# Kernel tuning notes

Measured on AMD Instinct MI355X. Metric: run time of the kernel, lower is better.

Reference implementation:

```python
import jax, jax.numpy as jnp
import numpy as np

V, E, M, L = 32000, 1024, 4096, 4  # vocab, embed_dim, mlp_dim, mlp_layers
B, S = 4, 2048                      # batch, seq_len


def setup_inputs() -> dict:
    key = jax.random.key(0)
    ks = jax.random.split(key, 7)
    init = lambda k, shape, fan: (jax.random.normal(k, shape, jnp.float32) / np.sqrt(fan).astype(np.float32))
    return {
        "x": jax.random.randint(ks[0], (B, S), 0, V),
        "emb": init(ks[1], (V, E), E),
        "Wq": init(ks[2], (E, E), E), "bq": jnp.zeros((E,), jnp.float32),
        "Wk": init(ks[3], (E, E), E), "bk": jnp.zeros((E,), jnp.float32),
        "Wv": init(ks[4], (E, E), E), "bv": jnp.zeros((E,), jnp.float32),
        "W1": init(ks[5], (L, E, M), E), "b1": jnp.zeros((L, M), jnp.float32),
        "W2": init(ks[6], (L, M, E), M), "b2": jnp.zeros((L, E), jnp.float32),
    }


def reference(x, emb, Wq, bq, Wk, bk, Wv, bv, W1, b1, W2, b2):
    h = emb[x]                                   # [B,S,E]
    q = h @ Wq + bq
    k = h @ Wk + bk
    v = h @ Wv + bv
    scale = 1.0 / np.sqrt(E).astype(np.float32)
    scores = jnp.einsum("bse,bte->bst", q, k) * scale   # [B,S,S]
    # torch.triu(ones, diagonal=0): keep upper triangle incl. diagonal (anti-causal/suffix mask)
    mask = jnp.triu(jnp.ones((S, S), dtype=bool), k=0)
    scores = jnp.where(mask, scores, -jnp.inf)
    w = jax.nn.softmax(scores, axis=-1)
    h = jax.nn.relu(jnp.einsum("bst,bte->bse", w, v))
    for i in range(L):
        h = jax.nn.relu(h @ W1[i] + b1[i])
        h = jax.nn.relu(h @ W2[i] + b2[i])
    return h
```

## Files before the change

### kernel.cpp

```cpp
#include <hip/hip_runtime.h>
#include <hip/hip_bf16.h>

#define EDIM 1024
#define MDIM 4096
#define SEQ  2048
#define NB   4
#define ROWS 8192

#define BM 128
#define BN 128
#define BK 32

typedef short bh8 __attribute__((ext_vector_type(8)));
typedef float f32x16 __attribute__((ext_vector_type(16)));

__device__ __forceinline__ float bf2f(unsigned short u) {
    return __uint_as_float(((unsigned int)u) << 16);
}
__device__ __forceinline__ unsigned short f2bf(float f) {
    unsigned int u = __float_as_uint(f);
    u += 0x7FFFu + ((u >> 16) & 1u);
    return (unsigned short)(u >> 16);
}
__device__ __forceinline__ void splitf(float v, unsigned short& h, unsigned short& l) {
    h = f2bf(v);
    l = f2bf(v - __uint_as_float(((unsigned int)h) << 16));
}
__device__ __forceinline__ void ld4f(const float* __restrict__ p, float* d) {
    const float4 v = *reinterpret_cast<const float4*>(p);
    d[0] = v.x; d[1] = v.y; d[2] = v.z; d[3] = v.w;
}
__device__ __forceinline__ void ld4h(const unsigned short* __restrict__ p, float* d) {
    const ushort4 v = *reinterpret_cast<const ushort4*>(p);
    d[0] = bf2f(v.x); d[1] = bf2f(v.y); d[2] = bf2f(v.z); d[3] = bf2f(v.w);
}

__device__ __forceinline__ long long tidx8(int n, int k, int KD16) {
    return ((((long long)(n >> 5) * KD16 + (k >> 4)) * 2 + ((k >> 3) & 1)) * 32 + (n & 31)) * 8;
}

__global__ __launch_bounds__(64)
void sniff_k(const unsigned int* __restrict__ w, int* __restrict__ flag) {
    int ok = 0;
    const int base = threadIdx.x * 32;
#pragma unroll
    for (int i = 0; i < 32; ++i) {
        const unsigned int v = w[base + i];
        const unsigned int lo = v & 0xFFFFu, hi = v >> 16;
        const unsigned int el = (lo >> 7) & 0xFF, eh = (hi >> 7) & 0xFF;
        const bool okl = (lo == 0u) || (el >= 0x30u && el <= 0x7Eu);
        const bool okh = (hi == 0u) || (eh >= 0x30u && eh <= 0x7Eu);
        ok += (okl && okh) ? 1 : 0;
    }
#pragma unroll
    for (int off = 32; off > 0; off >>= 1) ok += __shfl_down(ok, off);
    if (threadIdx.x == 0) *flag = (ok > 1400) ? 1 : 0;
}

__global__ __launch_bounds__(256)
void gather_k(const int* __restrict__ x, const void* __restrict__ emb,
              float* __restrict__ h, const int* __restrict__ flagp) {
    const int bf = *flagp;
    const long long row = blockIdx.x;
    const int idx = x[row];
    const long long off = (long long)idx * EDIM + threadIdx.x * 4;
    float d[4];
    if (bf) ld4h((const unsigned short*)emb + off, d);
    else    ld4f((const float*)emb + off, d);
    *reinterpret_cast<float4*>(h + row * EDIM + threadIdx.x * 4)
        = make_float4(d[0], d[1], d[2], d[3]);
}

__global__ __launch_bounds__(256)
void splitrows_tiled_k(const float* __restrict__ in, unsigned short* __restrict__ oh,
                       unsigned short* __restrict__ ol) {
    const int rr = blockIdx.x * 2 + (threadIdx.x >> 7);
    const int chunk = threadIdx.x & 127;
    const int k = chunk * 8;
    const float* p = in + (long long)rr * 1024 + k;
    float d[8];
    ld4f(p, d); ld4f(p + 4, d + 4);
    unsigned short h[8], l[8];
#pragma unroll
    for (int j = 0; j < 8; ++j) splitf(d[j], h[j], l[j]);
    const int z = rr >> 11, n = rr & 2047;
    const long long o = (long long)z * (2048LL * 1024) + tidx8(n, k, 64);
    uint4 hv, lv;
    hv.x = (unsigned)h[0] | ((unsigned)h[1] << 16);
    hv.y = (unsigned)h[2] | ((unsigned)h[3] << 16);
    hv.z = (unsigned)h[4] | ((unsigned)h[5] << 16);
    hv.w = (unsigned)h[6] | ((unsigned)h[7] << 16);
    lv.x = (unsigned)l[0] | ((unsigned)l[1] << 16);
    lv.y = (unsigned)l[2] | ((unsigned)l[3] << 16);
    lv.z = (unsigned)l[4] | ((unsigned)l[5] << 16);
    lv.w = (unsigned)l[6] | ((unsigned)l[7] << 16);
    *reinterpret_cast<uint4*>(oh + o) = hv;
    *reinterpret_cast<uint4*>(ol + o) = lv;
}

__global__ __launch_bounds__(256)
void splitT_tiled_k(const void* __restrict__ in, unsigned short* __restrict__ oh,
                    unsigned short* __restrict__ ol, int Kd, int Nd,
                    long long inOff, long long zIn, long long zOut,
                    const int* __restrict__ flagp, int bF) {
    const int bf = bF ? *flagp : 0;
    const long long ib = inOff + (long long)blockIdx.z * zIn;
    const long long ob = (long long)blockIdx.z * zOut;
    const int k0 = blockIdx.y * 32, n0 = blockIdx.x * 32;
    const int KD16 = Kd >> 4;
    __shared__ float t[32][33];
    const int c = threadIdx.x & 31, r0 = threadIdx.x >> 5;
#pragma unroll
    for (int i = 0; i < 4; ++i) {
        const int r = r0 + i * 8;
        const long long off = ib + (long long)(k0 + r) * Nd + n0 + c;
        t[r][c] = bf ? bf2f(((const unsigned short*)in)[off]) : ((const float*)in)[off];
    }
    __syncthreads();
#pragma unroll
    for (int i = 0; i < 4; ++i) {
        const int r = r0 + i * 8;
        const float v = t[c][r];
        unsigned short hh, ll;
        splitf(v, hh, ll);
        const int n = n0 + r, k = k0 + c;
        const long long oo = ob + tidx8(n, k, KD16) + (k & 7);
        oh[oo] = hh; ol[oo] = ll;
    }
}

template<bool BIAS, bool RELU, bool MASK>
__global__ __launch_bounds__(256, 3)
void mgemm_k(const float* __restrict__ A,
             const unsigned short* __restrict__ Bh,
             const unsigned short* __restrict__ Bl,
             const void* __restrict__ biasv, void* __restrict__ Cv,
             int M, int N, int K,
             long long sA, long long sB, long long sC,
             long long biasBase, float scale,
             const int* __restrict__ flagp, int bF, int cF) {
    const int flag = *flagp;
    const int bfBias = bF ? flag : 0;
    const int bfC = cF ? flag : 0;

    A  += (long long)blockIdx.z * sA;
    Bh += (long long)blockIdx.z * sB;
    Bl += (long long)blockIdx.z * sB;
    const long long zC = (long long)blockIdx.z * sC;

    const int GX = gridDim.x;
    const int f = blockIdx.y * GX + blockIdx.x;
    const int gxpc = GX >> 3;
    const int xcd = f & 7, p = f >> 3;
    const int bx = xcd * gxpc + (p % gxpc);
    const int by = p / gxpc;
    const int brow = by * BM, bcol = bx * BN;

    const int tid = threadIdx.x;
    const int lane = tid & 63, wave = tid >> 6;
    const int wr = wave >> 1, wc = wave & 1;
    const int l31 = lane & 31, lhi = lane >> 5;

    if (MASK && (bcol + BN - 1 < brow)) {
#pragma unroll
        for (int mi = 0; mi < 2; ++mi) {
            const int rbase = brow + wr * 64 + mi * 32 + 4 * lhi;
#pragma unroll
            for (int ni = 0; ni < 2; ++ni) {
                const int c = bcol + wc * 64 + ni * 32 + l31;
#pragma unroll
                for (int e = 0; e < 16; ++e) {
                    const int r = rbase + (e & 3) + 8 * (e >> 2);
                    ((float*)Cv)[zC + (long long)r * N + c] = -1e30f;
                }
            }
        }
        return;
    }

    __shared__ __align__(16) unsigned short Ash[2][BM * BK];
    __shared__ __align__(16) unsigned short Asl[2][BM * BK];

    f32x16 acc[2][2];
#pragma unroll
    for (int a = 0; a < 2; ++a)
#pragma unroll
        for (int b = 0; b < 2; ++b)
#pragma unroll
            for (int e = 0; e < 16; ++e) acc[a][b][e] = 0.f;

    const int arow = tid >> 3;
    const int akq  = (tid & 7) * 4;
    const int ablk = (tid & 7) >> 1;
    const int asub = (tid & 1) * 8;
    const float* Ap = A + (long long)(brow + arow) * K + akq;

    const int KD16 = K >> 4;
    const long long bbase0 = ((long long)((bcol >> 5) + wc * 2 + 0) * KD16) * 512 + lane * 8;
    const long long bbase1 = ((long long)((bcol >> 5) + wc * 2 + 1) * KD16) * 512 + lane * 8;

    float4 areg[4];
    bh8 b0[4], b1[4];

    auto loadA = [&](int k0) {
#pragma unroll
        for (int i = 0; i < 4; ++i)
            areg[i] = *reinterpret_cast<const float4*>(Ap + (long long)32 * i * K + k0);
    };
    auto stageA = [&](int b) {
#pragma unroll
        for (int i = 0; i < 4; ++i) {
            const int m = arow + 32 * i;
            const int byt = m * 64 + ((ablk ^ (m & 3)) << 4) + asub;
            unsigned short h0, h1, h2, h3, l0, l1, l2, l3;
            splitf(areg[i].x, h0, l0); splitf(areg[i].y, h1, l1);
            splitf(areg[i].z, h2, l2); splitf(areg[i].w, h3, l3);
            uint2 hp, lp;
            hp.x = (unsigned)h0 | ((unsigned)h1 << 16);
            hp.y = (unsigned)h2 | ((unsigned)h3 << 16);
            lp.x = (unsigned)l0 | ((unsigned)l1 << 16);
            lp.y = (unsigned)l2 | ((unsigned)l3 << 16);
            *reinterpret_cast<uint2*>(reinterpret_cast<char*>(&Ash[b][0]) + byt) = hp;
            *reinterpret_cast<uint2*>(reinterpret_cast<char*>(&Asl[b][0]) + byt) = lp;
        }
    };

#define LOADB(dst, k4v) { \
    const long long kk_ = (long long)(k4v) * 512; \
    dst[0] = *reinterpret_cast<const bh8*>(Bh + bbase0 + kk_); \
    dst[1] = *reinterpret_cast<const bh8*>(Bh + bbase1 + kk_); \
    dst[2] = *reinterpret_cast<const bh8*>(Bl + bbase0 + kk_); \
    dst[3] = *reinterpret_cast<const bh8*>(Bl + bbase1 + kk_); }

#define AFRAG(dsth, dstl, MI) { \
    const int r_ = wr * 64 + (MI) * 32 + l31; \
    const int byt_ = r_ * 64 + ((kb ^ (r_ & 3)) << 4); \
    dsth = *reinterpret_cast<const bh8*>(reinterpret_cast<const char*>(&Ash[bufc][0]) + byt_); \
    dstl = *reinterpret_cast<const bh8*>(reinterpret_cast<const char*>(&Asl[bufc][0]) + byt_); }

#define COMPUTE_KS(KS, BS) { \
    const int kb = (KS) * 2 + lhi; \
    bh8 ah0, al0, ah1, al1; \
    AFRAG(ah0, al0, 0); AFRAG(ah1, al1, 1); \
    acc[0][0] = __builtin_amdgcn_mfma_f32_32x32x16_bf16(ah0, BS[0], acc[0][0], 0, 0, 0); \
    acc[0][1] = __builtin_amdgcn_mfma_f32_32x32x16_bf16(ah0, BS[1], acc[0][1], 0, 0, 0); \
    acc[1][0] = __builtin_amdgcn_mfma_f32_32x32x16_bf16(ah1, BS[0], acc[1][0], 0, 0, 0); \
    acc[1][1] = __builtin_amdgcn_mfma_f32_32x32x16_bf16(ah1, BS[1], acc[1][1], 0, 0, 0); \
    acc[0][0] = __builtin_amdgcn_mfma_f32_32x32x16_bf16(ah0, BS[2], acc[0][0], 0, 0, 0); \
    acc[0][1] = __builtin_amdgcn_mfma_f32_32x32x16_bf16(ah0, BS[3], acc[0][1], 0, 0, 0); \
    acc[1][0] = __builtin_amdgcn_mfma_f32_32x32x16_bf16(ah1, BS[2], acc[1][0], 0, 0, 0); \
    acc[1][1] = __builtin_amdgcn_mfma_f32_32x32x16_bf16(ah1, BS[3], acc[1][1], 0, 0, 0); \
    acc[0][0] = __builtin_amdgcn_mfma_f32_32x32x16_bf16(al0, BS[0], acc[0][0], 0, 0, 0); \
    acc[0][1] = __builtin_amdgcn_mfma_f32_32x32x16_bf16(al0, BS[1], acc[0][1], 0, 0, 0); \
    acc[1][0] = __builtin_amdgcn_mfma_f32_32x32x16_bf16(al1, BS[0], acc[1][0], 0, 0, 0); \
    acc[1][1] = __builtin_amdgcn_mfma_f32_32x32x16_bf16(al1, BS[1], acc[1][1], 0, 0, 0); }

    const int NT = K >> 5;
    loadA(0);
    LOADB(b0, 0);
    LOADB(b1, 1);
    stageA(0);
    __syncthreads();
    loadA(32);

    for (int t = 0; t < NT; ++t) {
        const int bufc = t & 1;
        const int k4a = (2 * t + 2 < KD16) ? 2 * t + 2 : KD16 - 1;
        const int k4b = (2 * t + 3 < KD16) ? 2 * t + 3 : KD16 - 1;
        __builtin_amdgcn_s_setprio(1);
        COMPUTE_KS(0, b0);
        LOADB(b0, k4a);
        COMPUTE_KS(1, b1);
        LOADB(b1, k4b);
        __builtin_amdgcn_s_setprio(0);
        if (t + 1 < NT) {
            stageA((t + 1) & 1);
            __syncthreads();
            if (t + 2 < NT) loadA((t + 2) << 5);
        }
    }

#undef LOADB
#undef AFRAG
#undef COMPUTE_KS

#pragma unroll
    for (int mi = 0; mi < 2; ++mi) {
        const int rbase = brow + wr * 64 + mi * 32 + 4 * lhi;
#pragma unroll
        for (int ni = 0; ni < 2; ++ni) {
            const int c = bcol + wc * 64 + ni * 32 + l31;
            float bv = 0.f;
            if (BIAS) {
                const long long bo = biasBase + c;
                bv = bfBias ? bf2f(((const unsigned short*)biasv)[bo])
                            : ((const float*)biasv)[bo];
            }
#pragma unroll
            for (int e = 0; e < 16; ++e) {
                const int r = rbase + (e & 3) + 8 * (e >> 2);
                float v = acc[mi][ni][e];
                if (BIAS) v += bv;
                if (MASK) v = (c >= r) ? v * scale : -1e30f;
                if (RELU) v = fmaxf(v, 0.f);
                const long long off = zC + (long long)r * N + c;
                if (bfC) ((__hip_bfloat16*)Cv)[off] = __float2bfloat16(v);
                else     ((float*)Cv)[off] = v;
            }
        }
    }
}

__global__ __launch_bounds__(256)
void softmax_k(float* __restrict__ Sc) {
    float* row = Sc + (long long)blockIdx.y * SEQ * SEQ + (long long)blockIdx.x * SEQ;
    const int tid = threadIdx.x;

    float v[8];
    float m = -1e30f;
#pragma unroll
    for (int i = 0; i < 8; ++i) { v[i] = row[tid + i * 256]; m = fmaxf(m, v[i]); }
#pragma unroll
    for (int off = 32; off > 0; off >>= 1) m = fmaxf(m, __shfl_down(m, off));

    __shared__ float sm[4];
    __shared__ float ss[4];
    const int wid = tid >> 6, lane = tid & 63;
    if (lane == 0) sm[wid] = m;
    __syncthreads();
    const float mAll = fmaxf(fmaxf(sm[0], sm[1]), fmaxf(sm[2], sm[3]));

    float s = 0.f;
#pragma unroll
    for (int i = 0; i < 8; ++i) { v[i] = __expf(v[i] - mAll); s += v[i]; }
#pragma unroll
    for (int off = 32; off > 0; off >>= 1) s += __shfl_down(s, off);
    if (lane == 0) ss[wid] = s;
    __syncthreads();
    const float inv = 1.f / (ss[0] + ss[1] + ss[2] + ss[3]);
#pragma unroll
    for (int i = 0; i < 8; ++i) row[tid + i * 256] = v[i] * inv;
}

extern "C" void kernel_launch(void* const* d_in, const int* in_sizes, int n_in,
                              void* d_out, int out_size, void* d_ws, size_t ws_size,
                              hipStream_t stream) {
    const int*  x   = (const int*)d_in[0];
    const void* emb = d_in[1];
    const void* Wq  = d_in[2];
    const void* bq  = d_in[3];
    const void* Wk  = d_in[4];
    const void* bk  = d_in[5];
    const void* Wv  = d_in[6];
    const void* bv  = d_in[7];
    const void* W1  = d_in[8];
    const void* b1  = d_in[9];
    const void* W2  = d_in[10];
    const void* b2  = d_in[11];

    char* ws = (char*)d_ws;
    const long long SZ = 33554432LL;
    float* h    = (float*)(ws);
    float* q    = (float*)(ws + SZ);
    float* kx   = (float*)(ws + 2 * SZ);
    float* vx   = (float*)(ws + 3 * SZ);
    float* sc   = (float*)(ws + 3 * SZ);
    float* mid  = h;
    float* pong = (float*)(ws + 4 * SZ);
    float* att  = (float*)(ws + 6 * SZ);
    unsigned short* vxs_h = (unsigned short*)(ws + 2 * SZ);
    unsigned short* vxs_l = vxs_h + 8388608;
    unsigned short* kxs_h = (unsigned short*)(ws + 5 * SZ);
    unsigned short* kxs_l = kxs_h + 8388608;
    unsigned short* wslq_h = (unsigned short*)(ws + 4 * SZ);
    unsigned short* wslq_l = wslq_h + 1048576;
    unsigned short* wsl_h = (unsigned short*)(ws + 5 * SZ);
    unsigned short* wsl_l = wsl_h + 4194304;
    int* flag = (int*)(ws + 7 * SZ);

    const dim3 b256(256);
    const long long SE = (long long)SEQ * EDIM;
    const long long SS = (long long)SEQ * SEQ;
    const long long TSE = 2097152LL;

    sniff_k<<<1, 64, 0, stream>>>((const unsigned int*)emb, flag);
    gather_k<<<ROWS, b256, 0, stream>>>(x, emb, h, flag);

    splitT_tiled_k<<<dim3(32, 32, 1), b256, 0, stream>>>(
        Wq, wslq_h, wslq_l, EDIM, EDIM, 0, 0, 0, flag, 1);
    mgemm_k<true, false, false><<<dim3(EDIM / BN, ROWS / BM, 1), b256, 0, stream>>>(
        h, wslq_h, wslq_l, bq, q, ROWS, EDIM, EDIM, 0, 0, 0, 0, 1.f, flag, 1, 0);
    splitT_tiled_k<<<dim3(32, 32, 1), b256, 0, stream>>>(
        Wk, wslq_h, wslq_l, EDIM, EDIM, 0, 0, 0, flag, 1);
    mgemm_k<true, false, false><<<dim3(EDIM / BN, ROWS / BM, 1), b256, 0, stream>>>(
        h, wslq_h, wslq_l, bk, kx, ROWS, EDIM, EDIM, 0, 0, 0, 0, 1.f, flag, 1, 0);
    splitT_tiled_k<<<dim3(32, 32, 1), b256, 0, stream>>>(
        Wv, wslq_h, wslq_l, EDIM, EDIM, 0, 0, 0, flag, 1);
    mgemm_k<true, false, false><<<dim3(EDIM / BN, ROWS / BM, 1), b256, 0, stream>>>(
        h, wslq_h, wslq_l, bv, vx, ROWS, EDIM, EDIM, 0, 0, 0, 0, 1.f, flag, 1, 0);

    splitrows_tiled_k<<<ROWS / 2, b256, 0, stream>>>(kx, kxs_h, kxs_l);
    splitT_tiled_k<<<dim3(32, 64, NB), b256, 0, stream>>>(
        vx, vxs_h, vxs_l, SEQ, EDIM, 0, SE, TSE, flag, 0);

    mgemm_k<false, false, true><<<dim3(SEQ / BN, SEQ / BM, NB), b256, 0, stream>>>(
        q, kxs_h, kxs_l, nullptr, sc, SEQ, SEQ, EDIM, SE, TSE, SS, 0, 0.03125f, flag, 0, 0);

    softmax_k<<<dim3(SEQ, NB), b256, 0, stream>>>(sc);

    mgemm_k<false, true, false><<<dim3(EDIM / BN, SEQ / BM, NB), b256, 0, stream>>>(
        sc, vxs_h, vxs_l, nullptr, att, SEQ, EDIM, SEQ, SS, TSE, SE, 0, 1.f, flag, 0, 0);

    const float* cur = att;
    for (int i = 0; i < 4; ++i) {
        splitT_tiled_k<<<dim3(128, 32, 1), b256, 0, stream>>>(
            W1, wsl_h, wsl_l, EDIM, MDIM, (long long)i * EDIM * MDIM, 0, 0, flag, 1);
        mgemm_k<true, true, false><<<dim3(MDIM / BN, ROWS / BM, 1), b256, 0, stream>>>(
            cur, wsl_h, wsl_l, b1, mid, ROWS, MDIM, EDIM, 0, 0, 0,
            (long long)i * MDIM, 1.f, flag, 1, 0);

        splitT_tiled_k<<<dim3(32, 128, 1), b256, 0, stream>>>(
            W2, wsl_h, wsl_l, MDIM, EDIM, (long long)i * MDIM * EDIM, 0, 0, flag, 1);
        if (i < 3) {
            float* out = (cur == att) ? pong : att;
            mgemm_k<true, true, false><<<dim3(EDIM / BN, ROWS / BM, 1), b256, 0, stream>>>(
                mid, wsl_h, wsl_l, b2, out, ROWS, EDIM, MDIM, 0, 0, 0,
                (long long)i * EDIM, 1.f, flag, 1, 0);
            cur = out;
        } else {
            mgemm_k<true, true, false><<<dim3(EDIM / BN, ROWS / BM, 1), b256, 0, stream>>>(
                mid, wsl_h, wsl_l, b2, d_out, ROWS, EDIM, MDIM, 0, 0, 0,
                (long long)i * EDIM, 1.f, flag, 1, 1);
        }
    }
}
```

Baseline: 2.486 ms.

## Store activations pre-split in swizzled bf16 hi/lo layout and async-load A tiles

```diff
diff --git a/kernel.cpp b/kernel.cpp
--- a/kernel.cpp
+++ b/kernel.cpp
@@ -9,7 +9,6 @@
 
 #define BM 128
 #define BN 128
-#define BK 32
 
 typedef short bh8 __attribute__((ext_vector_type(8)));
 typedef float f32x16 __attribute__((ext_vector_type(16)));
@@ -35,8 +34,21 @@
     d[0] = bf2f(v.x); d[1] = bf2f(v.y); d[2] = bf2f(v.z); d[3] = bf2f(v.w);
 }
 
+__device__ __forceinline__ void async_copy16(void* lds, const void* g) {
+    __builtin_amdgcn_global_load_lds(
+        (const __attribute__((address_space(1))) unsigned int*)g,
+        (__attribute__((address_space(3))) unsigned int*)lds, 16, 0, 0);
+}
+
 __device__ __forceinline__ long long tidx8(int n, int k, int KD16) {
     return ((((long long)(n >> 5) * KD16 + (k >> 4)) * 2 + ((k >> 3) & 1)) * 32 + (n & 31)) * 8;
+}
+
+__device__ __forceinline__ void awrite(unsigned short* __restrict__ A, long long rc,
+                                       int r, int k, unsigned short h, unsigned short l) {
+    const int sub = (k & 31) >> 3, kb = k & 7, rx = r & 7;
+    A[rc + ((sub ^ rx) << 3) + kb] = h;
+    A[rc + (((4 + sub) ^ rx) << 3) + kb] = l;
 }
 
 __global__ __launch_bounds__(64)
@@ -59,53 +71,29 @@
 
 __global__ __launch_bounds__(256)
 void gather_k(const int* __restrict__ x, const void* __restrict__ emb,
-              float* __restrict__ h, const int* __restrict__ flagp) {
+              unsigned short* __restrict__ hA, const int* __restrict__ flagp) {
     const int bf = *flagp;
-    const long long row = blockIdx.x;
+    const int row = blockIdx.x;
     const int idx = x[row];
-    const long long off = (long long)idx * EDIM + threadIdx.x * 4;
+    const int k = threadIdx.x * 4;
+    const long long off = (long long)idx * EDIM + k;
     float d[4];
     if (bf) ld4h((const unsigned short*)emb + off, d);
     else    ld4f((const float*)emb + off, d);
-    *reinterpret_cast<float4*>(h + row * EDIM + threadIdx.x * 4)
-        = make_float4(d[0], d[1], d[2], d[3]);
-}
-
-__global__ __launch_bounds__(256)
-void splitrows_tiled_k(const float* __restrict__ in, unsigned short* __restrict__ oh,
-                       unsigned short* __restrict__ ol) {
-    const int rr = blockIdx.x * 2 + (threadIdx.x >> 7);
-    const int chunk = threadIdx.x & 127;
-    const int k = chunk * 8;
-    const float* p = in + (long long)rr * 1024 + k;
-    float d[8];
-    ld4f(p, d); ld4f(p + 4, d + 4);
-    unsigned short h[8], l[8];
-#pragma unroll
-    for (int j = 0; j < 8; ++j) splitf(d[j], h[j], l[j]);
-    const int z = rr >> 11, n = rr & 2047;
-    const long long o = (long long)z * (2048LL * 1024) + tidx8(n, k, 64);
-    uint4 hv, lv;
-    hv.x = (unsigned)h[0] | ((unsigned)h[1] << 16);
-    hv.y = (unsigned)h[2] | ((unsigned)h[3] << 16);
-    hv.z = (unsigned)h[4] | ((unsigned)h[5] << 16);
-    hv.w = (unsigned)h[6] | ((unsigned)h[7] << 16);
-    lv.x = (unsigned)l[0] | ((unsigned)l[1] << 16);
-    lv.y = (unsigned)l[2] | ((unsigned)l[3] << 16);
-    lv.z = (unsigned)l[4] | ((unsigned)l[5] << 16);
-    lv.w = (unsigned)l[6] | ((unsigned)l[7] << 16);
-    *reinterpret_cast<uint4*>(oh + o) = hv;
-    *reinterpret_cast<uint4*>(ol + o) = lv;
+    unsigned short h0, l0, h1, l1, h2, l2, h3, l3;
+    splitf(d[0], h0, l0); splitf(d[1], h1, l1);
+    splitf(d[2], h2, l2); splitf(d[3], h3, l3);
+    const int rx = row & 7, sub = (k & 31) >> 3, kb = k & 7;
+    const long long rc = ((long long)row * 32 + (k >> 5)) * 64;
+    *reinterpret_cast<ushort4*>(hA + rc + ((sub ^ rx) << 3) + kb) = make_ushort4(h0, h1, h2, h3);
+    *reinterpret_cast<ushort4*>(hA + rc + (((4 + sub) ^ rx) << 3) + kb) = make_ushort4(l0, l1, l2, l3);
 }
 
 __global__ __launch_bounds__(256)
 void splitT_tiled_k(const void* __restrict__ in, unsigned short* __restrict__ oh,
                     unsigned short* __restrict__ ol, int Kd, int Nd,
-                    long long inOff, long long zIn, long long zOut,
-                    const int* __restrict__ flagp, int bF) {
+                    long long inOff, const int* __restrict__ flagp, int bF) {
     const int bf = bF ? *flagp : 0;
-    const long long ib = inOff + (long long)blockIdx.z * zIn;
-    const long long ob = (long long)blockIdx.z * zOut;
     const int k0 = blockIdx.y * 32, n0 = blockIdx.x * 32;
     const int KD16 = Kd >> 4;
     __shared__ float t[32][33];
@@ -113,7 +101,7 @@
 #pragma unroll
     for (int i = 0; i < 4; ++i) {
         const int r = r0 + i * 8;
-        const long long off = ib + (long long)(k0 + r) * Nd + n0 + c;
+        const long long off = inOff + (long long)(k0 + r) * Nd + n0 + c;
         t[r][c] = bf ? bf2f(((const unsigned short*)in)[off]) : ((const float*)in)[off];
     }
     __syncthreads();
@@ -124,20 +112,21 @@
         unsigned short hh, ll;
         splitf(v, hh, ll);
         const int n = n0 + r, k = k0 + c;
-        const long long oo = ob + tidx8(n, k, KD16) + (k & 7);
+        const long long oo = tidx8(n, k, KD16) + (k & 7);
         oh[oo] = hh; ol[oo] = ll;
     }
 }
 
-template<bool BIAS, bool RELU, bool MASK>
+template<int OM, bool BIAS, bool RELU, bool MASK>
 __global__ __launch_bounds__(256, 3)
-void mgemm_k(const float* __restrict__ A,
+void mgemm_k(const unsigned short* __restrict__ A,
              const unsigned short* __restrict__ Bh,
              const unsigned short* __restrict__ Bl,
-             const void* __restrict__ biasv, void* __restrict__ Cv,
+             const void* __restrict__ biasv,
+             void* __restrict__ Cv, void* __restrict__ Cv2,
              int M, int N, int K,
              long long sA, long long sB, long long sC,
-             long long biasBase, float scale,
+             long long biasBase, float scale, int oKD16, long long zOut,
              const int* __restrict__ flagp, int bF, int cF) {
     const int flag = *flagp;
     const int bfBias = bF ? flag : 0;
@@ -178,8 +167,7 @@
         return;
     }
 
-    __shared__ __align__(16) unsigned short Ash[2][BM * BK];
-    __shared__ __align__(16) unsigned short Asl[2][BM * BK];
+    __shared__ __align__(16) char Ash[2][BM * 128];
 
     f32x16 acc[2][2];
 #pragma unroll
@@ -189,39 +177,22 @@
 #pragma unroll
             for (int e = 0; e < 16; ++e) acc[a][b][e] = 0.f;
 
-    const int arow = tid >> 3;
-    const int akq  = (tid & 7) * 4;
-    const int ablk = (tid & 7) >> 1;
-    const int asub = (tid & 1) * 8;
-    const float* Ap = A + (long long)(brow + arow) * K + akq;
-
+    const int CH = K >> 5;
     const int KD16 = K >> 4;
+
     const long long bbase0 = ((long long)((bcol >> 5) + wc * 2 + 0) * KD16) * 512 + lane * 8;
     const long long bbase1 = ((long long)((bcol >> 5) + wc * 2 + 1) * KD16) * 512 + lane * 8;
 
-    float4 areg[4];
     bh8 b0[4], b1[4];
 
-    auto loadA = [&](int k0) {
-#pragma unroll
-        for (int i = 0; i < 4; ++i)
-            areg[i] = *reinterpret_cast<const float4*>(Ap + (long long)32 * i * K + k0);
-    };
-    auto stageA = [&](int b) {
+    auto stageA = [&](int buf, int chunk) {
+        char* lb = &Ash[buf][0] + tid * 16;
+        const char* gb = (const char*)A;
 #pragma unroll
         for (int i = 0; i < 4; ++i) {
-            const int m = arow + 32 * i;
-            const int byt = m * 64 + ((ablk ^ (m & 3)) << 4) + asub;
-            unsigned short h0, h1, h2, h3, l0, l1, l2, l3;
-            splitf(areg[i].x, h0, l0); splitf(areg[i].y, h1, l1);
-            splitf(areg[i].z, h2, l2); splitf(areg[i].w, h3, l3);
-            uint2 hp, lp;
-            hp.x = (unsigned)h0 | ((unsigned)h1 << 16);
-            hp.y = (unsigned)h2 | ((unsigned)h3 << 16);
-            lp.x = (unsigned)l0 | ((unsigned)l1 << 16);
-            lp.y = (unsigned)l2 | ((unsigned)l3 << 16);
-            *reinterpret_cast<uint2*>(reinterpret_cast<char*>(&Ash[b][0]) + byt) = hp;
-            *reinterpret_cast<uint2*>(reinterpret_cast<char*>(&Asl[b][0]) + byt) = lp;
+            const int m = (tid >> 3) + i * 32;
+            const long long src = (((long long)(brow + m) * CH + chunk) << 7) + ((tid & 7) << 4);
+            async_copy16(lb + i * 4096, gb + src);
         }
     };
 
@@ -234,9 +205,9 @@
 
 #define AFRAG(dsth, dstl, MI) { \
     const int r_ = wr * 64 + (MI) * 32 + l31; \
-    const int byt_ = r_ * 64 + ((kb ^ (r_ & 3)) << 4); \
-    dsth = *reinterpret_cast<const bh8*>(reinterpret_cast<const char*>(&Ash[bufc][0]) + byt_); \
-    dstl = *reinterpret_cast<const bh8*>(reinterpret_cast<const char*>(&Asl[bufc][0]) + byt_); }
+    const char* base_ = &Ash[bufc][0] + r_ * 128; \
+    dsth = *reinterpret_cast<const bh8*>(base_ + (((kb) ^ (r_ & 7)) << 4)); \
+    dstl = *reinterpret_cast<const bh8*>(base_ + (((4 + kb) ^ (r_ & 7)) << 4)); }
 
 #define COMPUTE_KS(KS, BS) { \
     const int kb = (KS) * 2 + lhi; \
@@ -255,16 +226,15 @@
     acc[1][0] = __builtin_amdgcn_mfma_f32_32x32x16_bf16(al1, BS[0], acc[1][0], 0, 0, 0); \
     acc[1][1] = __builtin_amdgcn_mfma_f32_32x32x16_bf16(al1, BS[1], acc[1][1], 0, 0, 0); }
 
-    const int NT = K >> 5;
-    loadA(0);
+    const int NT = CH;
     LOADB(b0, 0);
     LOADB(b1, 1);
-    stageA(0);
+    stageA(0, 0);
     __syncthreads();
-    loadA(32);
 
     for (int t = 0; t < NT; ++t) {
         const int bufc = t & 1;
+        if (t + 1 < NT) stageA((t + 1) & 1, t + 1);
         const int k4a = (2 * t + 2 < KD16) ? 2 * t + 2 : KD16 - 1;
         const int k4b = (2 * t + 3 < KD16) ? 2 * t + 3 : KD16 - 1;
         __builtin_amdgcn_s_setprio(1);
@@ -273,11 +243,7 @@
         COMPUTE_KS(1, b1);
         LOADB(b1, k4b);
         __builtin_amdgcn_s_setprio(0);
-        if (t + 1 < NT) {
-            stageA((t + 1) & 1);
-            __syncthreads();
-            if (t + 2 < NT) loadA((t + 2) << 5);
-        }
+        __syncthreads();
     }
 
 #undef LOADB
@@ -296,37 +262,78 @@
                 bv = bfBias ? bf2f(((const unsigned short*)biasv)[bo])
                             : ((const float*)biasv)[bo];
             }
-#pragma unroll
-            for (int e = 0; e < 16; ++e) {
-                const int r = rbase + (e & 3) + 8 * (e >> 2);
-                float v = acc[mi][ni][e];
-                if (BIAS) v += bv;
-                if (MASK) v = (c >= r) ? v * scale : -1e30f;
-                if (RELU) v = fmaxf(v, 0.f);
-                const long long off = zC + (long long)r * N + c;
-                if (bfC) ((__hip_bfloat16*)Cv)[off] = __float2bfloat16(v);
-                else     ((float*)Cv)[off] = v;
+            if constexpr (OM == 3) {
+#pragma unroll
+                for (int g = 0; g < 4; ++g) {
+                    const int t0 = rbase + 8 * g;
+                    const int z = t0 >> 11, tt = t0 & 2047;
+                    float vv[4];
+#pragma unroll
+                    for (int d = 0; d < 4; ++d) {
+                        float v = acc[mi][ni][g * 4 + d];
+                        if (BIAS) v += bv;
+                        if (RELU) v = fmaxf(v, 0.f);
+                        vv[d] = v;
+                    }
+                    unsigned short h0, l0, h1, l1, h2, l2, h3, l3;
+                    splitf(vv[0], h0, l0); splitf(vv[1], h1, l1);
+                    splitf(vv[2], h2, l2); splitf(vv[3], h3, l3);
+                    const long long o = (long long)z * zOut +
+                        (((long long)(c >> 5) * oKD16 + (tt >> 4)) * 2 + ((tt >> 3) & 1)) * 256 +
+                        (c & 31) * 8 + (tt & 7);
+                    *reinterpret_cast<ushort4*>((unsigned short*)Cv + o) = make_ushort4(h0, h1, h2, h3);
+                    *reinterpret_cast<ushort4*>((unsigned short*)Cv2 + o) = make_ushort4(l0, l1, l2, l3);
+                }
+            } else {
+#pragma unroll
+                for (int e = 0; e < 16; ++e) {
+                    const int r = rbase + (e & 3) + 8 * (e >> 2);
+                    float v = acc[mi][ni][e];
+                    if (BIAS) v += bv;
+                    if (MASK) v = (c >= r) ? v * scale : -1e30f;
+                    if (RELU) v = fmaxf(v, 0.f);
+                    if constexpr (OM == 0) {
+                        const long long off = zC + (long long)r * N + c;
+                        if (bfC) ((__hip_bfloat16*)Cv)[off] = __float2bfloat16(v);
+                        else     ((float*)Cv)[off] = v;
+                    } else if constexpr (OM == 1) {
+                        unsigned short hh, ll;
+                        splitf(v, hh, ll);
+                        const long long rc = zC + ((long long)r * (N >> 5) + (c >> 5)) * 64;
+                        awrite((unsigned short*)Cv, rc, r, c, hh, ll);
+                    } else {
+                        unsigned short hh, ll;
+                        splitf(v, hh, ll);
+                        const int z = r >> 11, n = r & 2047;
+                        const long long o = (long long)z * zOut +
+                            (((long long)(n >> 5) * oKD16 + (c >> 4)) * 2 + ((c >> 3) & 1)) * 256 +
+                            (n & 31) * 8 + (c & 7);
+                        ((unsigned short*)Cv)[o] = hh;
+                        ((unsigned short*)Cv2)[o] = ll;
+                    }
+                }
             }
         }
     }
 }
 
 __global__ __launch_bounds__(256)
-void softmax_k(float* __restrict__ Sc) {
-    float* row = Sc + (long long)blockIdx.y * SEQ * SEQ + (long long)blockIdx.x * SEQ;
+void softmax_k(const float* __restrict__ Sc, unsigned short* __restrict__ W) {
+    const int m = blockIdx.x, z = blockIdx.y;
+    const float* row = Sc + ((long long)z * SEQ + m) * SEQ;
     const int tid = threadIdx.x;
 
     float v[8];
-    float m = -1e30f;
-#pragma unroll
-    for (int i = 0; i < 8; ++i) { v[i] = row[tid + i * 256]; m = fmaxf(m, v[i]); }
-#pragma unroll
-    for (int off = 32; off > 0; off >>= 1) m = fmaxf(m, __shfl_down(m, off));
+    float mx = -1e30f;
+#pragma unroll
+    for (int i = 0; i < 8; ++i) { v[i] = row[tid + i * 256]; mx = fmaxf(mx, v[i]); }
+#pragma unroll
+    for (int off = 32; off > 0; off >>= 1) mx = fmaxf(mx, __shfl_down(mx, off));
 
     __shared__ float sm[4];
     __shared__ float ss[4];
     const int wid = tid >> 6, lane = tid & 63;
-    if (lane == 0) sm[wid] = m;
+    if (lane == 0) sm[wid] = mx;
     __syncthreads();
     const float mAll = fmaxf(fmaxf(sm[0], sm[1]), fmaxf(sm[2], sm[3]));
 
@@ -338,8 +345,16 @@
     if (lane == 0) ss[wid] = s;
     __syncthreads();
     const float inv = 1.f / (ss[0] + ss[1] + ss[2] + ss[3]);
-#pragma unroll
-    for (int i = 0; i < 8; ++i) row[tid + i * 256] = v[i] * inv;
+
+    unsigned short* Wb = W + (long long)z * (SEQ * 4096LL);
+#pragma unroll
+    for (int i = 0; i < 8; ++i) {
+        const int k = tid + i * 256;
+        unsigned short hh, ll;
+        splitf(v[i] * inv, hh, ll);
+        const long long rc = ((long long)m * 64 + (k >> 5)) * 64;
+        awrite(Wb, rc, m, k, hh, ll);
+    }
 }
 
 extern "C" void kernel_launch(void* const* d_in, const int* in_sizes, int n_in,
@@ -360,77 +375,77 @@
 
     char* ws = (char*)d_ws;
     const long long SZ = 33554432LL;
-    float* h    = (float*)(ws);
-    float* q    = (float*)(ws + SZ);
-    float* kx   = (float*)(ws + 2 * SZ);
-    float* vx   = (float*)(ws + 3 * SZ);
-    float* sc   = (float*)(ws + 3 * SZ);
-    float* mid  = h;
-    float* pong = (float*)(ws + 4 * SZ);
-    float* att  = (float*)(ws + 6 * SZ);
-    unsigned short* vxs_h = (unsigned short*)(ws + 2 * SZ);
+    unsigned short* hA    = (unsigned short*)(ws);
+    unsigned short* qA    = (unsigned short*)(ws + SZ);
+    unsigned short* kxs_h = (unsigned short*)(ws + 2 * SZ);
+    unsigned short* kxs_l = kxs_h + 8388608;
+    unsigned short* vxs_h = (unsigned short*)(ws + 3 * SZ);
     unsigned short* vxs_l = vxs_h + 8388608;
-    unsigned short* kxs_h = (unsigned short*)(ws + 5 * SZ);
-    unsigned short* kxs_l = kxs_h + 8388608;
-    unsigned short* wslq_h = (unsigned short*)(ws + 4 * SZ);
-    unsigned short* wslq_l = wslq_h + 1048576;
-    unsigned short* wsl_h = (unsigned short*)(ws + 5 * SZ);
-    unsigned short* wsl_l = wsl_h + 4194304;
+    float*          sc    = (float*)(ws + 4 * SZ);
+    unsigned short* watt  = (unsigned short*)(ws);
+    unsigned short* att   = (unsigned short*)(ws + 4 * SZ);
+    unsigned short* wmlp  = (unsigned short*)(ws + 5 * SZ);
+    unsigned short* w1_h  = wmlp,              * w1_l = wmlp + 4194304;
+    unsigned short* w2_h  = wmlp + 8388608,    * w2_l = wmlp + 12582912;
+    unsigned short* mid   = (unsigned short*)(ws);
+    unsigned short* wqkv  = (unsigned short*)(ws + 6 * SZ);
+    unsigned short* wq_h = wqkv,           * wq_l = wqkv + 1048576;
+    unsigned short* wk_h = wqkv + 2097152, * wk_l = wqkv + 3145728;
+    unsigned short* wv_h = wqkv + 4194304, * wv_l = wqkv + 5242880;
+    unsigned short* out6  = (unsigned short*)(ws + 6 * SZ);
     int* flag = (int*)(ws + 7 * SZ);
 
     const dim3 b256(256);
-    const long long SE = (long long)SEQ * EDIM;
     const long long SS = (long long)SEQ * SEQ;
     const long long TSE = 2097152LL;
 
     sniff_k<<<1, 64, 0, stream>>>((const unsigned int*)emb, flag);
-    gather_k<<<ROWS, b256, 0, stream>>>(x, emb, h, flag);
-
-    splitT_tiled_k<<<dim3(32, 32, 1), b256, 0, stream>>>(
-        Wq, wslq_h, wslq_l, EDIM, EDIM, 0, 0, 0, flag, 1);
-    mgemm_k<true, false, false><<<dim3(EDIM / BN, ROWS / BM, 1), b256, 0, stream>>>(
-        h, wslq_h, wslq_l, bq, q, ROWS, EDIM, EDIM, 0, 0, 0, 0, 1.f, flag, 1, 0);
-    splitT_tiled_k<<<dim3(32, 32, 1), b256, 0, stream>>>(
-        Wk, wslq_h, wslq_l, EDIM, EDIM, 0, 0, 0, flag, 1);
-    mgemm_k<true, false, false><<<dim3(EDIM / BN, ROWS / BM, 1), b256, 0, stream>>>(
-        h, wslq_h, wslq_l, bk, kx, ROWS, EDIM, EDIM, 0, 0, 0, 0, 1.f, flag, 1, 0);
-    splitT_tiled_k<<<dim3(32, 32, 1), b256, 0, stream>>>(
-        Wv, wslq_h, wslq_l, EDIM, EDIM, 0, 0, 0, flag, 1);
-    mgemm_k<true, false, false><<<dim3(EDIM / BN, ROWS / BM, 1), b256, 0, stream>>>(
-        h, wslq_h, wslq_l, bv, vx, ROWS, EDIM, EDIM, 0, 0, 0, 0, 1.f, flag, 1, 0);
-
-    splitrows_tiled_k<<<ROWS / 2, b256, 0, stream>>>(kx, kxs_h, kxs_l);
-    splitT_tiled_k<<<dim3(32, 64, NB), b256, 0, stream>>>(
-        vx, vxs_h, vxs_l, SEQ, EDIM, 0, SE, TSE, flag, 0);
-
-    mgemm_k<false, false, true><<<dim3(SEQ / BN, SEQ / BM, NB), b256, 0, stream>>>(
-        q, kxs_h, kxs_l, nullptr, sc, SEQ, SEQ, EDIM, SE, TSE, SS, 0, 0.03125f, flag, 0, 0);
-
-    softmax_k<<<dim3(SEQ, NB), b256, 0, stream>>>(sc);
-
-    mgemm_k<false, true, false><<<dim3(EDIM / BN, SEQ / BM, NB), b256, 0, stream>>>(
-        sc, vxs_h, vxs_l, nullptr, att, SEQ, EDIM, SEQ, SS, TSE, SE, 0, 1.f, flag, 0, 0);
-
-    const float* cur = att;
+    gather_k<<<ROWS, b256, 0, stream>>>(x, emb, hA, flag);
+
+    splitT_tiled_k<<<dim3(32, 32, 1), b256, 0, stream>>>(Wq, wq_h, wq_l, EDIM, EDIM, 0, flag, 1);
+    splitT_tiled_k<<<dim3(32, 32, 1), b256, 0, stream>>>(Wk, wk_h, wk_l, EDIM, EDIM, 0, flag, 1);
+    splitT_tiled_k<<<dim3(32, 32, 1), b256, 0, stream>>>(Wv, wv_h, wv_l, EDIM, EDIM, 0, flag, 1);
+
+    mgemm_k<1, true, false, false><<<dim3(8, 64, 1), b256, 0, stream>>>(
+        hA, wq_h, wq_l, bq, qA, nullptr, ROWS, EDIM, EDIM,
+        0, 0, 0, 0, 1.f, 0, 0, flag, 1, 0);
+    mgemm_k<2, true, false, false><<<dim3(8, 64, 1), b256, 0, stream>>>(
+        hA, wk_h, wk_l, bk, kxs_h, kxs_l, ROWS, EDIM, EDIM,
+        0, 0, 0, 0, 1.f, 64, TSE, flag, 1, 0);
+    mgemm_k<3, true, false, false><<<dim3(8, 64, 1), b256, 0, stream>>>(
+        hA, wv_h, wv_l, bv, vxs_h, vxs_l, ROWS, EDIM, EDIM,
+        0, 0, 0, 0, 1.f, 128, TSE, flag, 1, 0);
+
+    mgemm_k<0, false, false, true><<<dim3(16, 16, NB), b256, 0, stream>>>(
+        qA, kxs_h, kxs_l, nullptr, sc, nullptr, SEQ, SEQ, EDIM,
+        4194304LL, TSE, SS, 0, 0.03125f, 0, 0, flag, 0, 0);
+
+    softmax_k<<<dim3(SEQ, NB), b256, 0, stream>>>(sc, watt);
+
+    mgemm_k<1, false, true, false><<<dim3(8, 16, NB), b256, 0, stream>>>(
+        watt, vxs_h, vxs_l, nullptr, att, nullptr, SEQ, EDIM, SEQ,
+        8388608LL, TSE, 4194304LL, 0, 1.f, 0, 0, flag, 0, 0);
+
+    const unsigned short* cur = att;
     for (int i = 0; i < 4; ++i) {
         splitT_tiled_k<<<dim3(128, 32, 1), b256, 0, stream>>>(
-            W1, wsl_h, wsl_l, EDIM, MDIM, (long long)i * EDIM * MDIM, 0, 0, flag, 1);
-        mgemm_k<true, true, false><<<dim3(MDIM / BN, ROWS / BM, 1), b256, 0, stream>>>(
-            cur, wsl_h, wsl_l, b1, mid, ROWS, MDIM, EDIM, 0, 0, 0,
-            (long long)i * MDIM, 1.f, flag, 1, 0);
+            W1, w1_h, w1_l, EDIM, MDIM, (long long)i * EDIM * MDIM, flag, 1);
+        mgemm_k<1, true, true, false><<<dim3(32, 64, 1), b256, 0, stream>>>(
+            cur, w1_h, w1_l, b1, mid, nullptr, ROWS, MDIM, EDIM,
+            0, 0, 0, (long long)i * MDIM, 1.f, 0, 0, flag, 1, 0);
 
         splitT_tiled_k<<<dim3(32, 128, 1), b256, 0, stream>>>(
-            W2, wsl_h, wsl_l, MDIM, EDIM, (long long)i * MDIM * EDIM, 0, 0, flag, 1);
+            W2, w2_h, w2_l, MDIM, EDIM, (long long)i * MDIM * EDIM, flag, 1);
         if (i < 3) {
-            float* out = (cur == att) ? pong : att;
-            mgemm_k<true, true, false><<<dim3(EDIM / BN, ROWS / BM, 1), b256, 0, stream>>>(
-                mid, wsl_h, wsl_l, b2, out, ROWS, EDIM, MDIM, 0, 0, 0,
-                (long long)i * EDIM, 1.f, flag, 1, 0);
+            unsigned short* out = (cur == att) ? out6 : att;
+            mgemm_k<1, true, true, false><<<dim3(8, 64, 1), b256, 0, stream>>>(
+                mid, w2_h, w2_l, b2, out, nullptr, ROWS, EDIM, MDIM,
+                0, 0, 0, (long long)i * EDIM, 1.f, 0, 0, flag, 1, 0);
             cur = out;
         } else {
-            mgemm_k<true, true, false><<<dim3(EDIM / BN, ROWS / BM, 1), b256, 0, stream>>>(
-                mid, wsl_h, wsl_l, b2, d_out, ROWS, EDIM, MDIM, 0, 0, 0,
-                (long long)i * EDIM, 1.f, flag, 1, 1);
+            mgemm_k<0, true, true, false><<<dim3(8, 64, 1), b256, 0, stream>>>(
+                mid, w2_h, w2_l, b2, d_out, nullptr, ROWS, EDIM, MDIM,
+                0, 0, 0, (long long)i * EDIM, 1.f, 0, 0, flag, 1, 1);
         }
     }
 }
```

Measured after the change: 2.314 ms. 6.9% less time.
